# Kernel tuning notes

Hardware: AMD Instinct MI355X
Metric: run time of the kernel (lower is better)

The kernel has to match this reference:

```python
import jax, jax.numpy as jnp
import numpy as np

# static sizes (see shape_source)
OBJ_N, WALL_N, FLOOR_N = 192, 16, 1
T = OBJ_N + WALL_N + FLOOR_N          # 209 total nodes
R = T * T - T                          # 43472 directed edges (no self loops)
D = 512
STEPS = 4                              # feat_update_step (1 group)
OBJ_IN, WALL_IN, FLOOR_IN, REL_IN = 42, 15, 16, 2

# buildMap: all-pairs meshgrid edges, self-loops removed, one-hot subj/obj maps
_nd = ~np.eye(T, dtype=bool)
_si, _oi = np.meshgrid(np.arange(T), np.arange(T), indexing='ij')
_subj_idx = _si[_nd]
_obj_idx = _oi[_nd]
SUBJ_MAP = jnp.asarray((np.arange(T)[:, None] == _subj_idx[None, :]).astype(np.float32))  # [T,R]
OBJ_MAP = jnp.asarray((np.arange(T)[:, None] == _obj_idx[None, :]).astype(np.float32))    # [T,R]
TOTAL_MAP = jnp.ones((T, T), jnp.float32)
REL_IDX = jnp.asarray(np.nonzero(_nd.reshape(-1))[0])  # [R] static gather indices


def setup_inputs():
    key = jax.random.key(0)
    ks = iter(jax.random.split(key, 64))
    def w(shape):
        return jax.random.normal(next(ks), shape, jnp.float32) * 0.01  # normal_(0, 0.01)
    inp = {
        'cat_object_feature': jax.random.normal(next(ks), (1, OBJ_N, OBJ_IN), jnp.float32),
        'cat_wall_feature': jax.random.normal(next(ks), (1, WALL_N, WALL_IN), jnp.float32),
        'cat_floor_feature': jax.random.normal(next(ks), (1, FLOOR_N, FLOOR_IN), jnp.float32),
        'cat_relation_feature': jax.random.normal(next(ks), (1, OBJ_N * OBJ_N, REL_IN), jnp.float32),
    }
    for name, din in [('obj', OBJ_IN), ('wall', WALL_IN), ('floor', FLOOR_IN), ('rel', REL_IN)]:
        inp[name + '_w1'] = w((din, D)); inp[name + '_b1'] = jnp.zeros((D,), jnp.float32)
        inp[name + '_w2'] = w((D, D));   inp[name + '_b2'] = jnp.zeros((D,), jnp.float32)
    inp['collect_w'] = w((5, D, D))                       # 5 _Collection_Unit fc weights
    inp['collect_b'] = jnp.zeros((5, D), jnp.float32)
    for name in ['tr', 'eu', 'sc']:
        inp[name + '_w1'] = w((D, D // 2)); inp[name + '_b1'] = jnp.zeros((D // 2,), jnp.float32)
        inp[name + '_w2'] = w((D // 2, 3)); inp[name + '_b2'] = jnp.zeros((3,), jnp.float32)
    return inp


def _mlp(x, w1, b1, w2, b2):
    return jax.nn.relu(x @ w1 + b1) @ w2 + b2


def _head(x, w1, b1, w2, b2):
    # Linear -> LeakyReLU(0.2) -> Dropout(eval: identity) -> Linear
    return jax.nn.leaky_relu(x @ w1 + b1, 0.2) @ w2 + b2


def _collect(src, attn, w, b):
    # _Collection_Unit: attn @ relu(fc(src)) / (row_sum + 1e-7)
    fc = jax.nn.relu(src @ w + b)
    return (attn @ fc) / (attn.sum(1, keepdims=True) + 1e-7)


def reference(cat_object_feature, cat_wall_feature, cat_floor_feature, cat_relation_feature,
              obj_w1, obj_b1, obj_w2, obj_b2, wall_w1, wall_b1, wall_w2, wall_b2,
              floor_w1, floor_b1, floor_w2, floor_b2, rel_w1, rel_b1, rel_w2, rel_b2,
              collect_w, collect_b, tr_w1, tr_b1, tr_w2, tr_b2,
              eu_w1, eu_b1, eu_w2, eu_b2, sc_w1, sc_b1, sc_w2, sc_b2):
    tot = jnp.concatenate([
        _mlp(cat_object_feature[0], obj_w1, obj_b1, obj_w2, obj_b2),
        _mlp(cat_wall_feature[0], wall_w1, wall_b1, wall_w2, wall_b2),
        _mlp(cat_floor_feature[0], floor_w1, floor_b1, floor_w2, floor_b2)], axis=0)  # [T,D]
    emb_rel = _mlp(cat_relation_feature[0], rel_w1, rel_b1, rel_w2, rel_b2)
    padded = jnp.pad(emb_rel.reshape(OBJ_N, OBJ_N, D),
                     ((0, T - OBJ_N), (0, T - OBJ_N), (0, 0)), constant_values=0.001)
    rel = padded.reshape(T * T, D)[REL_IDX]  # mask_total_relation_feature [R,D]

    for _ in range(STEPS):
        s_obj = _collect(tot, TOTAL_MAP, collect_w[4], collect_b[4])
        s_rs = _collect(rel, SUBJ_MAP, collect_w[0], collect_b[0])
        s_ro = _collect(rel, OBJ_MAP, collect_w[1], collect_b[1])
        new_tot = tot + (s_obj + s_rs + s_ro) / 3.0          # _Update_Unit: target + source
        s_os = _collect(tot, SUBJ_MAP.T, collect_w[2], collect_b[2])
        s_oo = _collect(tot, OBJ_MAP.T, collect_w[3], collect_b[3])
        rel = rel + (s_os + s_oo) / 2.0
        tot = new_tot

    obj = tot[:OBJ_N]  # object_mask select
    return jnp.concatenate([
        _head(obj, tr_w1, tr_b1, tr_w2, tr_b2),
        _head(obj, eu_w1, eu_b1, eu_w2, eu_b2),
        _head(obj, sc_w1, sc_b1, sc_w2, sc_b2)], axis=-1)  # [OBJ_N, 9]
```

## Files before the change

kernel.cpp:

```cpp
#include <hip/hip_runtime.h>
#include <stdint.h>

typedef unsigned short u16;
typedef __attribute__((ext_vector_type(4))) float f32x4;
typedef __attribute__((ext_vector_type(8))) short s16x8;
typedef __attribute__((ext_vector_type(4))) short s16x4;

#define DD (512*512)

__device__ inline u16 f2bf(float f) {
  uint32_t u = __float_as_uint(f);
  u = (u + 0x7FFFu + ((u >> 16) & 1u)) >> 16;
  return (u16)u;
}
__device__ inline float bflo(uint32_t w) { return __uint_as_float(w << 16); }
__device__ inline float bfhi(uint32_t w) { return __uint_as_float(w & 0xFFFF0000u); }
__device__ inline f32x4 relu4(f32x4 v) {
  f32x4 r;
  r.x = fmaxf(v.x, 0.f); r.y = fmaxf(v.y, 0.f);
  r.z = fmaxf(v.z, 0.f); r.w = fmaxf(v.w, 0.f);
  return r;
}
__device__ inline f32x4 bf4(const u16* p) {
  uint2 w = *(const uint2*)p;
  f32x4 r; r.x = bflo(w.x); r.y = bfhi(w.x); r.z = bflo(w.y); r.w = bfhi(w.y);
  return r;
}
__device__ inline s16x4 pack4(f32x4 v) {
  s16x4 o;
  o[0] = (short)f2bf(v.x); o[1] = (short)f2bf(v.y);
  o[2] = (short)f2bf(v.z); o[3] = (short)f2bf(v.w);
  return o;
}
__device__ inline void gload16(const void* g, void* l) {
  __builtin_amdgcn_global_load_lds(
      (const __attribute__((address_space(1))) void*)g,
      (__attribute__((address_space(3))) void*)l, 16, 0, 0);
}

__global__ __launch_bounds__(256) void ktotl1(const float* __restrict__ xo, const float* __restrict__ xw,
                                              const float* __restrict__ xf,
                                              const float* __restrict__ ow1, const float* __restrict__ ob1,
                                              const float* __restrict__ ww1, const float* __restrict__ wb1,
                                              const float* __restrict__ fw1, const float* __restrict__ fb1,
                                              float* __restrict__ hid) {
  int tc = blockIdx.x;
  const float* x; const float* w; const float* b; int K;
  if (tc < 192)      { x = xo + tc * 42;        w = ow1; b = ob1; K = 42; }
  else if (tc < 208) { x = xw + (tc - 192) * 15; w = ww1; b = wb1; K = 15; }
  else               { x = xf;                   w = fw1; b = fb1; K = 16; }
  __shared__ float xs[48];
  int t = threadIdx.x;
  if (t < K) xs[t] = x[t];
  __syncthreads();
  #pragma unroll
  for (int dd = 0; dd < 2; dd++) {
    int d = t + dd * 256;
    float acc = b[d];
    for (int k = 0; k < K; k++) acc = fmaf(xs[k], w[k * 512 + d], acc);
    hid[(size_t)tc * 512 + d] = fmaxf(acc, 0.f);
  }
}

struct SJob { const float* A; const float* B; const float* bias; float* C; u16* Cb; int M; int act; };
struct SJobs { SJob j[8]; int cum[9]; int njobs; };

__global__ __launch_bounds__(256) void ksmall(SJobs js) {
  int bi = blockIdx.x;
  int ji = 0;
  while (ji + 1 < js.njobs && bi >= js.cum[ji + 1]) ji++;
  SJob job = js.j[ji];
  int local = bi - js.cum[ji];
  int mt = local >> 3, nt = local & 7;
  int m0 = mt * 32, n0 = nt * 64;

  __shared__ float As[32 * 36];
  __shared__ float Bs[32 * 64];
  int t = threadIdx.x;
  int row = t >> 3;
  int cg  = (t & 7) * 8;
  f32x4 accA = {0.f,0.f,0.f,0.f}, accB = {0.f,0.f,0.f,0.f};

  for (int k0 = 0; k0 < 512; k0 += 32) {
    __syncthreads();
    {
      int ar = t >> 3, ac = (t & 7) * 4;
      f32x4 av = {0.f,0.f,0.f,0.f};
      if (m0 + ar < job.M) av = *(const f32x4*)&job.A[(size_t)(m0 + ar) * 512 + k0 + ac];
      *(f32x4*)&As[ar * 36 + ac] = av;
    }
    #pragma unroll
    for (int i = 0; i < 2; i++) {
      int idx = t + i * 256;
      int bk = idx >> 4, bn = (idx & 15) * 4;
      *(f32x4*)&Bs[bk * 64 + bn] = *(const f32x4*)&job.B[(size_t)(k0 + bk) * 512 + n0 + bn];
    }
    __syncthreads();
    #pragma unroll
    for (int kk = 0; kk < 32; kk += 4) {
      f32x4 a4 = *(const f32x4*)&As[row * 36 + kk];
      #pragma unroll
      for (int q = 0; q < 4; q++) {
        f32x4 b0 = *(const f32x4*)&Bs[(kk + q) * 64 + cg];
        f32x4 b1 = *(const f32x4*)&Bs[(kk + q) * 64 + cg + 4];
        float av = a4[q];
        accA += av * b0;
        accB += av * b1;
      }
    }
  }
  int r = m0 + row;
  if (r < job.M) {
    f32x4 b0 = {0.f,0.f,0.f,0.f}, b1 = {0.f,0.f,0.f,0.f};
    if (job.bias) { b0 = *(const f32x4*)&job.bias[n0 + cg]; b1 = *(const f32x4*)&job.bias[n0 + cg + 4]; }
    f32x4 o0 = accA + b0, o1 = accB + b1;
    if (job.act) { o0 = relu4(o0); o1 = relu4(o1); }
    *(f32x4*)&job.C[(size_t)r * 512 + n0 + cg]     = o0;
    *(f32x4*)&job.C[(size_t)r * 512 + n0 + cg + 4] = o1;
    if (job.Cb) {
      s16x8 ob;
      ob[0] = (short)f2bf(o0.x); ob[1] = (short)f2bf(o0.y);
      ob[2] = (short)f2bf(o0.z); ob[3] = (short)f2bf(o0.w);
      ob[4] = (short)f2bf(o1.x); ob[5] = (short)f2bf(o1.y);
      ob[6] = (short)f2bf(o1.z); ob[7] = (short)f2bf(o1.w);
      *(s16x8*)&job.Cb[(size_t)r * 512 + n0 + cg] = ob;
    }
  }
}

__global__ __launch_bounds__(256) void kcast(const float* __restrict__ src, u16* __restrict__ dst) {
  int g = blockIdx.x * 256 + threadIdx.x;
  f32x4 a = *(const f32x4*)&src[(size_t)g * 8];
  f32x4 b = *(const f32x4*)&src[(size_t)g * 8 + 4];
  s16x8 o;
  o[0] = (short)f2bf(a.x); o[1] = (short)f2bf(a.y); o[2] = (short)f2bf(a.z); o[3] = (short)f2bf(a.w);
  o[4] = (short)f2bf(b.x); o[5] = (short)f2bf(b.y); o[6] = (short)f2bf(b.z); o[7] = (short)f2bf(b.w);
  *(s16x8*)&dst[(size_t)g * 8] = o;
}

__global__ __launch_bounds__(256) void kwcast(const float* __restrict__ cw, u16* __restrict__ cwT) {
  __shared__ float tile[32][33];
  const float* src = cw + (size_t)blockIdx.z * DD;
  int k0 = blockIdx.x * 32, n0 = blockIdx.y * 32;
  int t = threadIdx.x;
  #pragma unroll
  for (int i = 0; i < 4; i++) {
    int idx = t + i * 256; int r = idx >> 5, c = idx & 31;
    tile[r][c] = src[(size_t)(k0 + r) * 512 + n0 + c];
  }
  __syncthreads();
  #pragma unroll
  for (int i = 0; i < 4; i++) {
    int idx = t + i * 256; int r = idx >> 5, c = idx & 31;
    cwT[((size_t)blockIdx.z * 512 + n0 + r) * 512 + k0 + c] = f2bf(tile[c][r]);
  }
}

__global__ __launch_bounds__(256) void kwct(const float* __restrict__ tmp0, const float* __restrict__ tmp1,
                                            u16* __restrict__ WcT) {
  __shared__ float tile[32][33];
  const float* src = blockIdx.z ? tmp1 : tmp0;
  int k0 = blockIdx.x * 32, n0 = blockIdx.y * 32;
  int t = threadIdx.x;
  #pragma unroll
  for (int i = 0; i < 4; i++) {
    int idx = t + i * 256; int r = idx >> 5, c = idx & 31;
    tile[r][c] = src[(size_t)(k0 + r) * 512 + n0 + c];
  }
  __syncthreads();
  #pragma unroll
  for (int i = 0; i < 4; i++) {
    int idx = t + i * 256; int r = idx >> 5, c = idx & 31;
    WcT[((size_t)blockIdx.z * 512 + n0 + r) * 512 + k0 + c] = f2bf(tile[c][r]);
  }
}

__global__ __launch_bounds__(256) void kmisc(const float* __restrict__ cw, const float* __restrict__ cb,
                                             const float* __restrict__ rb2,
                                             float* __restrict__ b0b, float* __restrict__ b0p,
                                             float* __restrict__ b1b, float* __restrict__ b1p) {
  int t = threadIdx.x;
  int dl = t & 63;
  int d = blockIdx.x * 64 + dl;
  int kg = t >> 6;
  const float* W0 = cw;
  const float* W1 = cw + DD;
  float a0 = 0, p0 = 0, a1 = 0, p1 = 0;
  for (int k = kg * 128; k < (kg + 1) * 128; ++k) {
    float w0 = W0[(size_t)k * 512 + d], w1 = W1[(size_t)k * 512 + d], r = rb2[k];
    a0 = fmaf(r, w0, a0); p0 += w0;
    a1 = fmaf(r, w1, a1); p1 += w1;
  }
  __shared__ float red[4][4][64];
  red[0][kg][dl] = a0; red[1][kg][dl] = p0; red[2][kg][dl] = a1; red[3][kg][dl] = p1;
  __syncthreads();
  if (kg == 0) {
    float s0  = red[0][0][dl] + red[0][1][dl] + red[0][2][dl] + red[0][3][dl];
    float sp0 = red[1][0][dl] + red[1][1][dl] + red[1][2][dl] + red[1][3][dl];
    float s1  = red[2][0][dl] + red[2][1][dl] + red[2][2][dl] + red[2][3][dl];
    float sp1 = red[3][0][dl] + red[3][1][dl] + red[3][2][dl] + red[3][3][dl];
    float bb0 = cb[0 * 512 + d], bb1 = cb[1 * 512 + d];
    b0b[d] = s0 + bb0;
    b0p[d] = 0.001f * sp0 + bb0;
    b1b[d] = s1 + bb1;
    b1p[d] = 0.001f * sp1 + bb1;
  }
}

__global__ __launch_bounds__(256) void kH(const float* __restrict__ xr, const float* __restrict__ rw1,
                                          const float* __restrict__ rb1, u16* __restrict__ Hh) {
  int gid = blockIdx.x * 256 + threadIdx.x;
  int m = gid >> 6;
  int dg = (gid & 63) * 8;
  float x0 = xr[m * 2], x1 = xr[m * 2 + 1];
  s16x8 o;
  #pragma unroll
  for (int j = 0; j < 8; j++) {
    int dd = dg + j;
    float v = fmaf(x0, rw1[dd], fmaf(x1, rw1[512 + dd], rb1[dd]));
    o[j] = (short)f2bf(fmaxf(v, 0.f));
  }
  *(s16x8*)&Hh[(size_t)m * 512 + dg] = o;
}

struct MJob { const u16* A; const u16* BT; const float* bias; float* C; int Mreal; int act; };
struct MJobs { MJob j[8]; int cum[9]; int njobs; };

__global__ __launch_bounds__(256) void kmg(MJobs js) {
  int bi = blockIdx.x;
  int ji = 0;
  while (ji + 1 < js.njobs && bi >= js.cum[ji + 1]) ji++;
  MJob job = js.j[ji];
  int local = bi - js.cum[ji];
  int m0 = (local >> 2) * 64, n0 = (local & 3) * 128;

  __shared__ u16 As[64 * 64];
  __shared__ u16 Bs[128 * 64];
  const int t = threadIdx.x;
  const int lane = t & 63;
  const int wave = t >> 6;
  const int wm = wave >> 1, wn = wave & 1;
  const int r16 = lane & 15;
  const int kq = lane >> 4;
  f32x4 acc[2][4];
  #pragma unroll
  for (int i = 0; i < 2; i++)
    #pragma unroll
    for (int j = 0; j < 4; j++) acc[i][j] = (f32x4){0.f,0.f,0.f,0.f};

  const u16* gA[2]; u16* lA[2];
  const u16* gB[4]; u16* lB[4];
  #pragma unroll
  for (int i = 0; i < 2; i++) {
    int seg = i * 256 + t;
    int row = seg >> 3, s = seg & 7;
    gA[i] = job.A + (size_t)(m0 + row) * 512 + ((s ^ (row & 7)) << 3);
    lA[i] = As + ((i * 256 + (t & 192)) << 3);
  }
  #pragma unroll
  for (int i = 0; i < 4; i++) {
    int seg = i * 256 + t;
    int row = seg >> 3, s = seg & 7;
    gB[i] = job.BT + (size_t)(n0 + row) * 512 + ((s ^ (row & 7)) << 3);
    lB[i] = Bs + ((i * 256 + (t & 192)) << 3);
  }

  for (int k0 = 0; k0 < 512; k0 += 64) {
    __syncthreads();
    #pragma unroll
    for (int i = 0; i < 2; i++) gload16(gA[i] + k0, lA[i]);
    #pragma unroll
    for (int i = 0; i < 4; i++) gload16(gB[i] + k0, lB[i]);
    __syncthreads();
    #pragma unroll
    for (int kh = 0; kh < 2; kh++) {
      s16x8 af[2], bfr[4];
      #pragma unroll
      for (int i = 0; i < 2; i++) {
        int r = wm * 32 + i * 16 + r16;
        af[i] = *(const s16x8*)&As[r * 64 + (((kq + kh * 4) ^ (r & 7)) << 3)];
      }
      #pragma unroll
      for (int j = 0; j < 4; j++) {
        int r = wn * 64 + j * 16 + r16;
        bfr[j] = *(const s16x8*)&Bs[r * 64 + (((kq + kh * 4) ^ (r & 7)) << 3)];
      }
      #pragma unroll
      for (int i = 0; i < 2; i++)
        #pragma unroll
        for (int j = 0; j < 4; j++)
          acc[i][j] = __builtin_amdgcn_mfma_f32_16x16x32_bf16(af[i], bfr[j], acc[i][j], 0, 0, 0);
    }
  }

  float bj[4] = {0.f, 0.f, 0.f, 0.f};
  if (job.bias) {
    #pragma unroll
    for (int j = 0; j < 4; j++) bj[j] = job.bias[n0 + wn * 64 + j * 16 + r16];
  }
  #pragma unroll
  for (int i = 0; i < 2; i++) {
    int rbase = m0 + wm * 32 + i * 16 + (lane >> 4) * 4;
    #pragma unroll
    for (int r = 0; r < 4; r++) {
      int grow = rbase + r;
      if (grow < job.Mreal) {
        #pragma unroll
        for (int j = 0; j < 4; j++) {
          float v = acc[i][j][r] + bj[j];
          if (job.act) v = fmaxf(v, 0.f);
          job.C[(size_t)grow * 512 + n0 + wn * 64 + j * 16 + r16] = v;
        }
      }
    }
  }
}

__global__ __launch_bounds__(256) void kbig(const u16* __restrict__ Hh, const u16* __restrict__ WcT,
                                            u16* __restrict__ Q0, u16* __restrict__ Q1T) {
  __shared__ u16 smem[2 * 128 * 64];
  u16* As = smem;
  u16* Bs = smem + 128 * 64;
  float* Cs = (float*)smem;
  const int m0 = blockIdx.x * 128;
  const int n0 = blockIdx.y * 128;
  const int t = threadIdx.x;
  const int lane = t & 63;
  const int wave = t >> 6;
  const int wm = wave >> 1, wn = wave & 1;
  const int r16 = lane & 15;
  const int kq = lane >> 4;
  f32x4 acc[4][4];
  #pragma unroll
  for (int i = 0; i < 4; i++)
    #pragma unroll
    for (int j = 0; j < 4; j++) acc[i][j] = (f32x4){0.f, 0.f, 0.f, 0.f};

  const u16* gA[4]; const u16* gB[4];
  u16* lA[4]; u16* lB[4];
  #pragma unroll
  for (int i = 0; i < 4; i++) {
    int seg = i * 256 + t;
    int row = seg >> 3, s = seg & 7;
    int sw = (s ^ (row & 7)) << 3;
    gA[i] = Hh  + (size_t)(m0 + row) * 512 + sw;
    gB[i] = WcT + (size_t)(n0 + row) * 512 + sw;
    int lbase = (i * 256 + (t & 192)) << 3;
    lA[i] = As + lbase;
    lB[i] = Bs + lbase;
  }

  for (int k0 = 0; k0 < 512; k0 += 64) {
    __syncthreads();
    #pragma unroll
    for (int i = 0; i < 4; i++) gload16(gA[i] + k0, lA[i]);
    #pragma unroll
    for (int i = 0; i < 4; i++) gload16(gB[i] + k0, lB[i]);
    __syncthreads();
    #pragma unroll
    for (int kh = 0; kh < 2; kh++) {
      s16x8 af[4], bfr[4];
      #pragma unroll
      for (int i = 0; i < 4; i++) {
        int r = wm * 64 + i * 16 + r16;
        af[i] = *(const s16x8*)&As[r * 64 + (((kq + kh * 4) ^ (r & 7)) << 3)];
      }
      #pragma unroll
      for (int j = 0; j < 4; j++) {
        int r = wn * 64 + j * 16 + r16;
        bfr[j] = *(const s16x8*)&Bs[r * 64 + (((kq + kh * 4) ^ (r & 7)) << 3)];
      }
      #pragma unroll
      for (int i = 0; i < 4; i++)
        #pragma unroll
        for (int j = 0; j < 4; j++)
          acc[i][j] = __builtin_amdgcn_mfma_f32_16x16x32_bf16(af[i], bfr[j], acc[i][j], 0, 0, 0);
    }
  }

  const bool isQ1 = (n0 >= 512);
  #pragma unroll
  for (int c = 0; c < 4; c++) {
    __syncthreads();
    if ((c >> 1) == wm) {
      const int cbase = (c & 1) * 32;
      #pragma unroll
      for (int ii = 0; ii < 2; ii++) {
        const int i = (cbase >> 4) + ii;
        #pragma unroll
        for (int j = 0; j < 4; j++) {
          #pragma unroll
          for (int r = 0; r < 4; r++) {
            int rrow = i * 16 + (lane >> 4) * 4 + r - cbase;
            int ccol = wn * 64 + j * 16 + r16;
            Cs[rrow * 128 + ccol] = acc[i][j][r];
          }
        }
      }
    }
    __syncthreads();
    const int row = t >> 3, cg = (t & 7) * 16;
    const int gm = m0 + c * 32 + row;
    s16x8 o0, o1;
    #pragma unroll
    for (int x = 0; x < 8; x++) o0[x] = (short)f2bf(Cs[row * 128 + cg + x]);
    #pragma unroll
    for (int x = 0; x < 8; x++) o1[x] = (short)f2bf(Cs[row * 128 + cg + 8 + x]);
    u16* dst;
    if (!isQ1) {
      dst = Q0 + (size_t)gm * 512 + (n0 + cg);
    } else {
      int s = gm / 192, o = gm - s * 192;
      dst = Q1T + ((size_t)o * 192 + s) * 512 + (n0 - 512 + cg);
    }
    *(s16x8*)dst = o0;
    *(s16x8*)(dst + 8) = o1;
  }
}

__global__ __launch_bounds__(128) void kpass(const u16* __restrict__ Q0, const u16* __restrict__ Q1T,
                                             const float* __restrict__ u0, const float* __restrict__ v0,
                                             const float* __restrict__ u1, const float* __restrict__ v1,
                                             const float* __restrict__ b0b, const float* __restrict__ b1b,
                                             const float* __restrict__ fc4,
                                             float* __restrict__ part, float* __restrict__ sobj) {
  int z = blockIdx.z;
  int t = threadIdx.x;
  if (z == 2) {
    if (blockIdx.y != 0 || blockIdx.x >= 4) return;
    int d = blockIdx.x * 128 + t;
    float s = 0.f;
    for (int r = 0; r < 209; ++r) s += fc4[(size_t)r * 512 + d];
    sobj[d] = s;
    return;
  }
  int so = blockIdx.x;
  if (so >= 192) return;
  int chunk = blockIdx.y;
  int d = t * 4;
  const u16* Q = z ? Q1T : Q0;
  const float* fixtab  = z ? v1 : u0;
  const float* looptab = z ? u1 : v0;
  const float* bb = z ? b1b : b0b;
  f32x4 fix = *(const f32x4*)&fixtab[(size_t)so * 512 + d] + *(const f32x4*)&bb[d];
  f32x4 acc = {0.f,0.f,0.f,0.f};
  const u16* qbase = Q + ((size_t)so * 192 + chunk * 48) * 512 + d;
  const float* lbase = looptab + (size_t)(chunk * 48) * 512 + d;
  #pragma unroll 4
  for (int r = 0; r < 48; ++r) {
    f32x4 qa = bf4(qbase + (size_t)r * 512);
    f32x4 vv = *(const f32x4*)(lbase + (size_t)r * 512);
    f32x4 val = qa + fix + vv;
    acc.x += fmaxf(val.x, 0.f); acc.y += fmaxf(val.y, 0.f);
    acc.z += fmaxf(val.z, 0.f); acc.w += fmaxf(val.w, 0.f);
  }
  *(f32x4*)&part[(((size_t)z * 209 + so) * 4 + chunk) * 512 + d] = acc;
}

__global__ __launch_bounds__(128) void kfinish(const u16* __restrict__ Q0, const u16* __restrict__ Q1T,
                                               const float* __restrict__ u0, const float* __restrict__ v0,
                                               const float* __restrict__ u1, const float* __restrict__ v1,
                                               const float* __restrict__ b0b, const float* __restrict__ b0p,
                                               const float* __restrict__ b1b, const float* __restrict__ b1p,
                                               const float* __restrict__ part, const float* __restrict__ sobj,
                                               const float* __restrict__ fcS, const float* __restrict__ fcO,
                                               float* __restrict__ tot, float* __restrict__ addS,
                                               float* __restrict__ addO,
                                               u16* __restrict__ totb, u16* __restrict__ aSb,
                                               u16* __restrict__ aOb) {
  int tt = blockIdx.x;
  int t = threadIdx.x;
  int d = t * 4;
  size_t rowoff = (size_t)tt * 512 + d;
  f32x4 u0r = *(const f32x4*)&u0[rowoff];
  f32x4 v0r = *(const f32x4*)&v0[rowoff];
  f32x4 u1r = *(const f32x4*)&u1[rowoff];
  f32x4 v1r = *(const f32x4*)&v1[rowoff];
  f32x4 B0B = *(const f32x4*)&b0b[d];
  f32x4 B0P = *(const f32x4*)&b0p[d];
  f32x4 B1B = *(const f32x4*)&b1b[d];
  f32x4 B1P = *(const f32x4*)&b1p[d];
  f32x4 srs = {0.f,0.f,0.f,0.f}, sro = {0.f,0.f,0.f,0.f};
  if (tt < 192) {
    #pragma unroll
    for (int c = 0; c < 4; c++) {
      srs += *(const f32x4*)&part[(((size_t)0 * 209 + tt) * 4 + c) * 512 + d];
      sro += *(const f32x4*)&part[(((size_t)1 * 209 + tt) * 4 + c) * 512 + d];
    }
    for (int o = 192; o < 209; o++) srs += relu4(B0P + u0r + *(const f32x4*)&v0[(size_t)o * 512 + d]);
    for (int s = 192; s < 209; s++) sro += relu4(B1P + *(const f32x4*)&u1[(size_t)s * 512 + d] + v1r);
    f32x4 qd0 = bf4(Q0 + ((size_t)tt * 193) * 512 + d);
    srs -= relu4(qd0 + u0r + v0r + B0B);
    f32x4 qd1 = bf4(Q1T + ((size_t)tt * 193) * 512 + d);
    sro -= relu4(qd1 + u1r + v1r + B1B);
  } else {
    for (int o = 0; o < 209; o++) srs += relu4(B0P + u0r + *(const f32x4*)&v0[(size_t)o * 512 + d]);
    srs -= relu4(B0P + u0r + v0r);
    for (int s = 0; s < 209; s++) sro += relu4(B1P + *(const f32x4*)&u1[(size_t)s * 512 + d] + v1r);
    sro -= relu4(B1P + u1r + v1r);
  }
  const float inv209 = 1.0f / (float)(209.0 + 1e-7);
  const float inv208 = 1.0f / (float)(208.0 + 1e-7);
  const float invrel = 0.5f / (float)(1.0 + 1e-7);
  f32x4 so4 = *(const f32x4*)&sobj[d] * inv209;
  srs *= inv208;
  sro *= inv208;
  f32x4 tt4 = *(const f32x4*)&tot[rowoff];
  tt4 += (so4 + srs + sro) * (1.0f / 3.0f);
  *(f32x4*)&tot[rowoff] = tt4;
  f32x4 aS = *(const f32x4*)&addS[rowoff] + *(const f32x4*)&fcS[rowoff] * invrel;
  f32x4 aO = *(const f32x4*)&addO[rowoff] + *(const f32x4*)&fcO[rowoff] * invrel;
  *(f32x4*)&addS[rowoff] = aS;
  *(f32x4*)&addO[rowoff] = aO;
  *(s16x4*)&totb[rowoff] = pack4(tt4);
  *(s16x4*)&aSb[rowoff]  = pack4(aS);
  *(s16x4*)&aOb[rowoff]  = pack4(aO);
}

__global__ __launch_bounds__(256) void kheads(const float* __restrict__ tot,
    const float* __restrict__ w1a, const float* __restrict__ b1a, const float* __restrict__ w2a, const float* __restrict__ b2a,
    const float* __restrict__ w1b, const float* __restrict__ b1bb, const float* __restrict__ w2b, const float* __restrict__ b2b,
    const float* __restrict__ w1c, const float* __restrict__ b1c, const float* __restrict__ w2c, const float* __restrict__ b2c,
    float* __restrict__ out) {
  int row = blockIdx.x;
  int t = threadIdx.x;
  __shared__ float xs[512];
  xs[t] = tot[(size_t)row * 512 + t];
  xs[t + 256] = tot[(size_t)row * 512 + 256 + t];
  __syncthreads();
  const float* W1[3] = {w1a, w1b, w1c};
  const float* B1[3] = {b1a, b1bb, b1c};
  const float* W2[3] = {w2a, w2b, w2c};
  float p[9];
  #pragma unroll
  for (int hd = 0; hd < 3; hd++) {
    float a = B1[hd][t];
    for (int k = 0; k < 512; k += 4) {
      f32x4 x4 = *(const f32x4*)&xs[k];
      a = fmaf(x4.x, W1[hd][(size_t)(k + 0) * 256 + t], a);
      a = fmaf(x4.y, W1[hd][(size_t)(k + 1) * 256 + t], a);
      a = fmaf(x4.z, W1[hd][(size_t)(k + 2) * 256 + t], a);
      a = fmaf(x4.w, W1[hd][(size_t)(k + 3) * 256 + t], a);
    }
    float h = a > 0.f ? a : 0.2f * a;
    p[hd * 3 + 0] = h * W2[hd][t * 3 + 0];
    p[hd * 3 + 1] = h * W2[hd][t * 3 + 1];
    p[hd * 3 + 2] = h * W2[hd][t * 3 + 2];
  }
  __shared__ float red[9][256];
  #pragma unroll
  for (int c = 0; c < 9; c++) red[c][t] = p[c];
  __syncthreads();
  for (int s = 128; s > 0; s >>= 1) {
    if (t < s) {
      #pragma unroll
      for (int c = 0; c < 9; c++) red[c][t] += red[c][t + s];
    }
    __syncthreads();
  }
  if (t < 9) {
    const float* B2[3] = {b2a, b2b, b2c};
    out[(size_t)row * 9 + t] = red[t][0] + B2[t / 3][t % 3];
  }
}

extern "C" void kernel_launch(void* const* d_in, const int* in_sizes, int n_in,
                              void* d_out, int out_size, void* d_ws, size_t ws_size,
                              hipStream_t stream) {
  const float* xo  = (const float*)d_in[0];
  const float* xw  = (const float*)d_in[1];
  const float* xf  = (const float*)d_in[2];
  const float* xr  = (const float*)d_in[3];
  const float* ow1 = (const float*)d_in[4];
  const float* ob1 = (const float*)d_in[5];
  const float* ow2 = (const float*)d_in[6];
  const float* ob2 = (const float*)d_in[7];
  const float* ww1 = (const float*)d_in[8];
  const float* wb1 = (const float*)d_in[9];
  const float* ww2 = (const float*)d_in[10];
  const float* wb2 = (const float*)d_in[11];
  const float* fw1 = (const float*)d_in[12];
  const float* fb1 = (const float*)d_in[13];
  const float* fw2 = (const float*)d_in[14];
  const float* fb2 = (const float*)d_in[15];
  const float* rw1 = (const float*)d_in[16];
  const float* rb1 = (const float*)d_in[17];
  const float* rw2 = (const float*)d_in[18];
  const float* rb2 = (const float*)d_in[19];
  const float* cw  = (const float*)d_in[20];
  const float* cb  = (const float*)d_in[21];
  const float* tw1 = (const float*)d_in[22];
  const float* tb1 = (const float*)d_in[23];
  const float* tw2 = (const float*)d_in[24];
  const float* tb2 = (const float*)d_in[25];
  const float* ew1 = (const float*)d_in[26];
  const float* eb1 = (const float*)d_in[27];
  const float* ew2 = (const float*)d_in[28];
  const float* eb2 = (const float*)d_in[29];
  const float* sw1 = (const float*)d_in[30];
  const float* sb1 = (const float*)d_in[31];
  const float* sw2 = (const float*)d_in[32];
  const float* sb2 = (const float*)d_in[33];
  float* out = (float*)d_out;

  char* p = (char*)d_ws;
  auto alloc = [&](size_t bytes) { char* r = p; p += (bytes + 255) & ~(size_t)255; return r; };
  const size_t SZ = 209 * 512 * sizeof(float);
  const size_t BSZ = 256 * 512 * sizeof(u16);
  float* tot  = (float*)alloc(SZ);
  float* addS = (float*)alloc(SZ);
  float* addO = (float*)alloc(SZ);
  u16*   totb = (u16*)alloc(BSZ);
  u16*   aSb  = (u16*)alloc(BSZ);
  u16*   aOb  = (u16*)alloc(BSZ);
  float* fc4  = (float*)alloc(SZ);
  float* fcS  = (float*)alloc(SZ);
  float* fcO  = (float*)alloc(SZ);
  float* u0   = (float*)alloc(SZ);
  float* v0   = (float*)alloc(SZ);
  float* u1   = (float*)alloc(SZ);
  float* v1   = (float*)alloc(SZ);
  float* hid  = (float*)alloc(SZ);
  float* sobj = (float*)alloc(512 * sizeof(float));
  float* part = (float*)alloc((size_t)2 * 209 * 4 * 512 * sizeof(float));
  float* b0b  = (float*)alloc(512 * sizeof(float));
  float* b0p  = (float*)alloc(512 * sizeof(float));
  float* b1b  = (float*)alloc(512 * sizeof(float));
  float* b1p  = (float*)alloc(512 * sizeof(float));
  float* tmp0 = (float*)alloc((size_t)DD * sizeof(float));
  float* tmp1 = (float*)alloc((size_t)DD * sizeof(float));
  u16* rw2b = (u16*)alloc((size_t)DD * sizeof(u16));
  u16* cwT  = (u16*)alloc((size_t)5 * DD * sizeof(u16));
  u16* Hh  = (u16*)alloc((size_t)36864 * 512 * sizeof(u16));
  u16* WcT = (u16*)alloc((size_t)1024 * 512 * sizeof(u16));
  u16* Q0  = (u16*)alloc((size_t)36864 * 512 * sizeof(u16));
  u16* Q1T = (u16*)alloc((size_t)36864 * 512 * sizeof(u16));

  hipMemsetAsync(addS, 0, 2 * SZ + 3 * BSZ, stream);

  ktotl1<<<209, 256, 0, stream>>>(xo, xw, xf, ow1, ob1, ww1, wb1, fw1, fb1, hid);
  kcast<<<128, 256, 0, stream>>>(rw2, rw2b);
  kwcast<<<dim3(16, 16, 5), 256, 0, stream>>>(cw, cwT);

  SJobs pre{};
  pre.j[0] = { hid,             ow2, ob2, tot,             totb,             192, 0 };
  pre.j[1] = { hid + 192 * 512, ww2, wb2, tot + 192 * 512, totb + 192 * 512,  16, 0 };
  pre.j[2] = { hid + 208 * 512, fw2, fb2, tot + 208 * 512, totb + 208 * 512,   1, 0 };
  pre.njobs = 3;
  pre.cum[0] = 0;
  for (int i = 0; i < 3; i++) pre.cum[i + 1] = pre.cum[i] + ((pre.j[i].M + 31) / 32) * 8;
  ksmall<<<pre.cum[3], 256, 0, stream>>>(pre);

  MJobs mpre{};
  mpre.j[0] = { rw2b, cwT,      nullptr, tmp0, 512, 0 };
  mpre.j[1] = { rw2b, cwT + DD, nullptr, tmp1, 512, 0 };
  mpre.njobs = 2;
  mpre.cum[0] = 0; mpre.cum[1] = 32; mpre.cum[2] = 64;
  kmg<<<64, 256, 0, stream>>>(mpre);

  kwct<<<dim3(16, 16, 2), 256, 0, stream>>>(tmp0, tmp1, WcT);
  kmisc<<<8, 256, 0, stream>>>(cw, cb, rb2, b0b, b0p, b1b, b1p);
  kH<<<9216, 256, 0, stream>>>(xr, rw1, rb1, Hh);
  kbig<<<dim3(288, 8), 256, 0, stream>>>(Hh, WcT, Q0, Q1T);

  MJobs st{};
  st.j[0] = { totb, cwT + 4 * DD, cb + 4 * 512, fc4, 209, 1 };
  st.j[1] = { totb, cwT + 2 * DD, cb + 2 * 512, fcS, 209, 1 };
  st.j[2] = { totb, cwT + 3 * DD, cb + 3 * 512, fcO, 209, 1 };
  st.j[3] = { aSb,  cwT,          nullptr,      u0,  209, 0 };
  st.j[4] = { aOb,  cwT,          nullptr,      v0,  209, 0 };
  st.j[5] = { aSb,  cwT + DD,     nullptr,      u1,  209, 0 };
  st.j[6] = { aOb,  cwT + DD,     nullptr,      v1,  209, 0 };
  st.njobs = 7;
  st.cum[0] = 0;
  for (int i = 0; i < 7; i++) st.cum[i + 1] = st.cum[i] + 4 * 4;

  for (int step = 0; step < 4; step++) {
    kmg<<<st.cum[7], 256, 0, stream>>>(st);
    kpass<<<dim3(209, 4, 3), 128, 0, stream>>>(Q0, Q1T, u0, v0, u1, v1, b0b, b1b, fc4, part, sobj);
    kfinish<<<209, 128, 0, stream>>>(Q0, Q1T, u0, v0, u1, v1, b0b, b0p, b1b, b1p,
                                     part, sobj, fcS, fcO, tot, addS, addO, totb, aSb, aOb);
  }

  kheads<<<192, 256, 0, stream>>>(tot, tw1, tb1, tw2, tb2, ew1, eb1, ew2, eb2, sw1, sb1, sw2, sb2, out);
}
```

Measured before the change: 452.4 us.

## Double-buffer LDS tiles in GEMM kernels, swap kbig grid order, pad epilogue

Both MFMA GEMM kernels (kmg and kbig) now use two LDS buffers. The next K-tile's global-to-LDS load is issued before computing on the current one, leaving one barrier per iteration instead of two. kbig's grid is transposed so blocks with the same M row-tile and different N tiles run next to each other, which should improve L2 reuse of the large Hh operand. The epilogue staging stride is padded from 128 to 132 floats to reduce LDS bank conflicts. The cost is double the LDS footprint (64KB for kbig), which may lower occupancy.

```diff
diff --git a/kernel.cpp b/kernel.cpp
--- a/kernel.cpp
+++ b/kernel.cpp
@@ -234,8 +234,7 @@
   int local = bi - js.cum[ji];
   int m0 = (local >> 2) * 64, n0 = (local & 3) * 128;
 
-  __shared__ u16 As[64 * 64];
-  __shared__ u16 Bs[128 * 64];
+  __shared__ u16 smem[2 * 12288];
   const int t = threadIdx.x;
   const int lane = t & 63;
   const int wave = t >> 6;
@@ -248,42 +247,53 @@
     #pragma unroll
     for (int j = 0; j < 4; j++) acc[i][j] = (f32x4){0.f,0.f,0.f,0.f};
 
-  const u16* gA[2]; u16* lA[2];
-  const u16* gB[4]; u16* lB[4];
+  const u16* gA[2]; int laofs[2];
+  const u16* gB[4]; int lbofs[4];
   #pragma unroll
   for (int i = 0; i < 2; i++) {
     int seg = i * 256 + t;
     int row = seg >> 3, s = seg & 7;
     gA[i] = job.A + (size_t)(m0 + row) * 512 + ((s ^ (row & 7)) << 3);
-    lA[i] = As + ((i * 256 + (t & 192)) << 3);
+    laofs[i] = (i * 256 + (t & 192)) << 3;
   }
   #pragma unroll
   for (int i = 0; i < 4; i++) {
     int seg = i * 256 + t;
     int row = seg >> 3, s = seg & 7;
     gB[i] = job.BT + (size_t)(n0 + row) * 512 + ((s ^ (row & 7)) << 3);
-    lB[i] = Bs + ((i * 256 + (t & 192)) << 3);
-  }
-
-  for (int k0 = 0; k0 < 512; k0 += 64) {
-    __syncthreads();
-    #pragma unroll
-    for (int i = 0; i < 2; i++) gload16(gA[i] + k0, lA[i]);
-    #pragma unroll
-    for (int i = 0; i < 4; i++) gload16(gB[i] + k0, lB[i]);
-    __syncthreads();
+    lbofs[i] = 4096 + ((i * 256 + (t & 192)) << 3);
+  }
+
+  #pragma unroll
+  for (int i = 0; i < 2; i++) gload16(gA[i], smem + laofs[i]);
+  #pragma unroll
+  for (int i = 0; i < 4; i++) gload16(gB[i], smem + lbofs[i]);
+  __syncthreads();
+
+  int buf = 0;
+  for (int it = 0; it < 8; ++it) {
+    if (it < 7) {
+      int nb = (buf ^ 1) * 12288;
+      int k0n = (it + 1) * 64;
+      #pragma unroll
+      for (int i = 0; i < 2; i++) gload16(gA[i] + k0n, smem + nb + laofs[i]);
+      #pragma unroll
+      for (int i = 0; i < 4; i++) gload16(gB[i] + k0n, smem + nb + lbofs[i]);
+    }
+    const u16* Ab = smem + buf * 12288;
+    const u16* Bb = Ab + 4096;
     #pragma unroll
     for (int kh = 0; kh < 2; kh++) {
       s16x8 af[2], bfr[4];
       #pragma unroll
       for (int i = 0; i < 2; i++) {
         int r = wm * 32 + i * 16 + r16;
-        af[i] = *(const s16x8*)&As[r * 64 + (((kq + kh * 4) ^ (r & 7)) << 3)];
+        af[i] = *(const s16x8*)&Ab[r * 64 + (((kq + kh * 4) ^ (r & 7)) << 3)];
       }
       #pragma unroll
       for (int j = 0; j < 4; j++) {
         int r = wn * 64 + j * 16 + r16;
-        bfr[j] = *(const s16x8*)&Bs[r * 64 + (((kq + kh * 4) ^ (r & 7)) << 3)];
+        bfr[j] = *(const s16x8*)&Bb[r * 64 + (((kq + kh * 4) ^ (r & 7)) << 3)];
       }
       #pragma unroll
       for (int i = 0; i < 2; i++)
@@ -291,6 +301,8 @@
         for (int j = 0; j < 4; j++)
           acc[i][j] = __builtin_amdgcn_mfma_f32_16x16x32_bf16(af[i], bfr[j], acc[i][j], 0, 0, 0);
     }
+    __syncthreads();
+    buf ^= 1;
   }
 
   float bj[4] = {0.f, 0.f, 0.f, 0.f};
@@ -318,12 +330,9 @@
 
 __global__ __launch_bounds__(256) void kbig(const u16* __restrict__ Hh, const u16* __restrict__ WcT,
                                             u16* __restrict__ Q0, u16* __restrict__ Q1T) {
-  __shared__ u16 smem[2 * 128 * 64];
-  u16* As = smem;
-  u16* Bs = smem + 128 * 64;
-  float* Cs = (float*)smem;
-  const int m0 = blockIdx.x * 128;
-  const int n0 = blockIdx.y * 128;
+  __shared__ u16 smem[2 * 16384];
+  const int m0 = blockIdx.y * 128;
+  const int n0 = blockIdx.x * 128;
   const int t = threadIdx.x;
   const int lane = t & 63;
   const int wave = t >> 6;
@@ -337,7 +346,7 @@
     for (int j = 0; j < 4; j++) acc[i][j] = (f32x4){0.f, 0.f, 0.f, 0.f};
 
   const u16* gA[4]; const u16* gB[4];
-  u16* lA[4]; u16* lB[4];
+  int lofs[4];
   #pragma unroll
   for (int i = 0; i < 4; i++) {
     int seg = i * 256 + t;
@@ -345,30 +354,41 @@
     int sw = (s ^ (row & 7)) << 3;
     gA[i] = Hh  + (size_t)(m0 + row) * 512 + sw;
     gB[i] = WcT + (size_t)(n0 + row) * 512 + sw;
-    int lbase = (i * 256 + (t & 192)) << 3;
-    lA[i] = As + lbase;
-    lB[i] = Bs + lbase;
-  }
-
-  for (int k0 = 0; k0 < 512; k0 += 64) {
-    __syncthreads();
-    #pragma unroll
-    for (int i = 0; i < 4; i++) gload16(gA[i] + k0, lA[i]);
-    #pragma unroll
-    for (int i = 0; i < 4; i++) gload16(gB[i] + k0, lB[i]);
-    __syncthreads();
+    lofs[i] = (i * 256 + (t & 192)) << 3;
+  }
+
+  #pragma unroll
+  for (int i = 0; i < 4; i++) {
+    gload16(gA[i], smem + lofs[i]);
+    gload16(gB[i], smem + 8192 + lofs[i]);
+  }
+  __syncthreads();
+
+  int buf = 0;
+  for (int it = 0; it < 8; ++it) {
+    if (it < 7) {
+      int nb = (buf ^ 1) * 16384;
+      int k0n = (it + 1) * 64;
+      #pragma unroll
+      for (int i = 0; i < 4; i++) {
+        gload16(gA[i] + k0n, smem + nb + lofs[i]);
+        gload16(gB[i] + k0n, smem + nb + 8192 + lofs[i]);
+      }
+    }
+    const u16* Ab = smem + buf * 16384;
+    const u16* Bb = Ab + 8192;
     #pragma unroll
     for (int kh = 0; kh < 2; kh++) {
       s16x8 af[4], bfr[4];
       #pragma unroll
       for (int i = 0; i < 4; i++) {
         int r = wm * 64 + i * 16 + r16;
-        af[i] = *(const s16x8*)&As[r * 64 + (((kq + kh * 4) ^ (r & 7)) << 3)];
+        af[i] = *(const s16x8*)&Ab[r * 64 + (((kq + kh * 4) ^ (r & 7)) << 3)];
       }
       #pragma unroll
       for (int j = 0; j < 4; j++) {
         int r = wn * 64 + j * 16 + r16;
-        bfr[j] = *(const s16x8*)&Bs[r * 64 + (((kq + kh * 4) ^ (r & 7)) << 3)];
+        bfr[j] = *(const s16x8*)&Bb[r * 64 + (((kq + kh * 4) ^ (r & 7)) << 3)];
       }
       #pragma unroll
       for (int i = 0; i < 4; i++)
@@ -376,8 +396,11 @@
         for (int j = 0; j < 4; j++)
           acc[i][j] = __builtin_amdgcn_mfma_f32_16x16x32_bf16(af[i], bfr[j], acc[i][j], 0, 0, 0);
     }
-  }
-
+    __syncthreads();
+    buf ^= 1;
+  }
+
+  float* Cs = (float*)smem;
   const bool isQ1 = (n0 >= 512);
   #pragma unroll
   for (int c = 0; c < 4; c++) {
@@ -393,7 +416,7 @@
           for (int r = 0; r < 4; r++) {
             int rrow = i * 16 + (lane >> 4) * 4 + r - cbase;
             int ccol = wn * 64 + j * 16 + r16;
-            Cs[rrow * 128 + ccol] = acc[i][j][r];
+            Cs[rrow * 132 + ccol] = acc[i][j][r];
           }
         }
       }
@@ -403,9 +426,9 @@
     const int gm = m0 + c * 32 + row;
     s16x8 o0, o1;
     #pragma unroll
-    for (int x = 0; x < 8; x++) o0[x] = (short)f2bf(Cs[row * 128 + cg + x]);
-    #pragma unroll
-    for (int x = 0; x < 8; x++) o1[x] = (short)f2bf(Cs[row * 128 + cg + 8 + x]);
+    for (int x = 0; x < 8; x++) o0[x] = (short)f2bf(Cs[row * 132 + cg + x]);
+    #pragma unroll
+    for (int x = 0; x < 8; x++) o1[x] = (short)f2bf(Cs[row * 132 + cg + 8 + x]);
     u16* dst;
     if (!isQ1) {
       dst = Q0 + (size_t)gm * 512 + (n0 + cg);
@@ -661,7 +684,7 @@
   kwct<<<dim3(16, 16, 2), 256, 0, stream>>>(tmp0, tmp1, WcT);
   kmisc<<<8, 256, 0, stream>>>(cw, cb, rb2, b0b, b0p, b1b, b1p);
   kH<<<9216, 256, 0, stream>>>(xr, rw1, rb1, Hh);
-  kbig<<<dim3(288, 8), 256, 0, stream>>>(Hh, WcT, Q0, Q1T);
+  kbig<<<dim3(8, 288), 256, 0, stream>>>(Hh, WcT, Q0, Q1T);
 
   MJobs st{};
   st.j[0] = { totb, cwT + 4 * DD, cb + 4 * 512, fc4, 209, 1 };
```

New measurement: 458.6 us. No clear change (+1.4%).
